# Kernel tuning notes

Hardware: AMD Instinct MI355X
Metric: run time of the kernel (lower is better)

## Reference

```python
import jax, jax.numpy as jnp
import numpy as np

B, N, IN_DIM, H, L = 8, 1024, 3, 256, 3
NUM_STEPS = 200
LN_EPS = 1e-5


def _cdist(a, b):
    # Euclidean pairwise distance, a:[B,n,d], b:[B,m,d] -> [B,n,m]
    d2 = (jnp.sum(a * a, -1)[:, :, None] + jnp.sum(b * b, -1)[:, None, :]
          - 2.0 * jnp.einsum('bik,bjk->bij', a, b))
    d2 = jnp.maximum(d2, 0.0)
    safe = jnp.sqrt(jnp.where(d2 > 0, d2, 1.0))
    return jnp.where(d2 > 0, safe, 0.0)


def _layernorm(x, g, b):
    mu = jnp.mean(x, -1, keepdims=True)
    var = jnp.mean(jnp.square(x - mu), -1, keepdims=True)
    return (x - mu) * jax.lax.rsqrt(var + LN_EPS) * g + b


def setup_inputs() -> dict:
    key = jax.random.key(0)
    ks = jax.random.split(key, 32)
    s = 0.02
    inp = {
        'x': jax.random.normal(ks[0], (B, N, IN_DIM), jnp.float32),
        't': jax.random.randint(ks[1], (B,), 0, NUM_STEPS),
        'mask': jnp.ones((B, N), bool),
        # top-level weights (stored [in,out])
        'w_time': jax.random.normal(ks[2], (1, H)) * s,
        'b_time': jnp.zeros((H,)),
        'w_in': jax.random.normal(ks[3], (IN_DIM + H, H)) * s,
        'b_in': jnp.zeros((H,)),
        'w_out': jax.random.normal(ks[4], (H, IN_DIM)) * s,
        'b_out': jnp.zeros((IN_DIM,)),
        # per-layer stacked params [L, ...]
        'qkv_w': jax.random.normal(ks[5], (L, H, 3 * H)) * s,
        'qkv_b': jnp.zeros((L, 3 * H)),
        'ao_w': jax.random.normal(ks[6], (L, H, H)) * s,
        'ao_b': jnp.zeros((L, H)),
        'fc1_w': jax.random.normal(ks[7], (L, H, 4 * H)) * s,
        'fc1_b': jax.random.normal(ks[8], (L, 4 * H)) * s,
        'fc2_w': jax.random.normal(ks[9], (L, 4 * H, H)) * s,
        'fc2_b': jax.random.normal(ks[10], (L, H)) * s,
        'ln1_g': jnp.ones((L, H)), 'ln1_b': jnp.zeros((L, H)),
        'ln2_g': jnp.ones((L, H)), 'ln2_b': jnp.zeros((L, H)),
    }
    return inp


def reference(x, t, mask, w_time, b_time, w_in, b_in, w_out, b_out,
              qkv_w, qkv_b, ao_w, ao_b, fc1_w, fc1_b, fc2_w, fc2_b,
              ln1_g, ln1_b, ln2_g, ln2_b):
    tf = t.astype(jnp.float32)[:, None] / float(NUM_STEPS)          # [B,1]
    t_embed = jax.nn.relu(tf @ w_time + b_time)                      # [B,H]
    t_embed = jnp.broadcast_to(t_embed[:, None, :], (B, N, H))
    h = jax.nn.relu(jnp.concatenate([x, t_embed], -1) @ w_in + b_in)  # [B,N,H]
    geo = _cdist(h[:, :, :3], h[:, :, :3])                           # [B,N,N]
    mask_f = mask.astype(h.dtype)
    scale = 1.0 / jnp.sqrt(jnp.float32(H))
    for l in range(L):
        qkv = (h @ qkv_w[l] + qkv_b[l]).reshape(B, N, 3, H)
        q, k, v = qkv[:, :, 0], qkv[:, :, 1], qkv[:, :, 2]
        dist = _cdist(geo, geo)                                      # cdist of the distance matrix itself
        scores = jnp.einsum('bik,bjk->bij', q, k) * scale * jnp.exp(-dist)
        scores = jnp.where(mask[:, None, :], scores, -jnp.inf)
        attn = jax.nn.softmax(scores, axis=-1)
        ao = (jnp.einsum('bij,bjk->bik', attn, v) @ ao_w[l] + ao_b[l]) * mask_f[:, :, None]
        xx = _layernorm(h + ao, ln1_g[l], ln1_b[l])
        f1 = jax.nn.relu((xx @ fc1_w[l] + fc1_b[l]) * mask_f[:, :, None])
        ffn = jax.nn.relu((f1 @ fc2_w[l] + fc2_b[l]) * mask_f[:, :, None])
        h = _layernorm(xx + ffn, ln2_g[l], ln2_b[l])
    return (h @ w_out + b_out) * mask_f[:, :, None]
```

## Files before the change

### kernel.cpp

```cpp
#include <hip/hip_runtime.h>
#include <math.h>

#define NB 8
#define NN 1024
#define NH 256
#define NL 3

typedef unsigned short u16;
typedef __bf16 bf16x8 __attribute__((ext_vector_type(8)));
typedef _Float16 f16x8 __attribute__((ext_vector_type(8)));
typedef float f32x4 __attribute__((ext_vector_type(4)));

constexpr int EPI_BIAS_RELU = 2, EPI_BIAS_RELU_RESID = 3, EPI_EDIST = 5, EPI_QKV = 6;

__device__ __forceinline__ unsigned bf16rne(float f) {
    unsigned u = __float_as_uint(f);
    return (u + 0x7fffu + ((u >> 16) & 1u)) >> 16;
}
__device__ __forceinline__ unsigned bfpair(float a, float b) {
    return bf16rne(a) | (bf16rne(b) << 16);
}
__device__ __forceinline__ float bf2f(u16 h) {
    unsigned u = ((unsigned)h) << 16;
    return __uint_as_float(u);
}

__device__ __forceinline__ float blockSum256(float v) {
    __shared__ float sm[4];
    #pragma unroll
    for (int o = 32; o; o >>= 1) v += __shfl_down(v, o, 64);
    int lane = threadIdx.x & 63, wid = threadIdx.x >> 6;
    if (lane == 0) sm[wid] = v;
    __syncthreads();
    if (threadIdx.x == 0) sm[0] = sm[0] + sm[1] + sm[2] + sm[3];
    __syncthreads();
    float r = sm[0];
    __syncthreads();
    return r;
}

template <int EPI, int DT, bool OBF, int SWZ, int MT>
__global__ __launch_bounds__(256) void gemm_mfma(
    const u16* __restrict__ A, int lda, long sA,
    const u16* __restrict__ Bt, int ldb, long sB,
    void* __restrict__ C, int ldc, long sC,
    int K,
    const float* __restrict__ bias, long sBias,
    const float* __restrict__ resid, int ldr,
    u16* __restrict__ vtout)
{
    constexpr int MF = MT / 32;
    constexpr int ASZ = MT * 8;
    __shared__ uint4 sm4[ASZ + 1024];
    const int tid = threadIdx.x;

    int bx = blockIdx.x, by = blockIdx.y, bz = blockIdx.z;
    bool trans = false;
    if (SWZ == 2) {
        int gx = gridDim.x;
        int T = gx * gridDim.y;
        int lid = bx + gx * by;
        int nl = (lid & 7) * (T >> 3) + (lid >> 3);
        bx = nl % gx; by = nl / gx;
    } else if (SWZ == 3) {
        int lid = bx + gridDim.x * bz;
        bz = lid & 7;
        int idx = lid >> 3;
        int j = 0;
        while (idx >= 16 - 2 * j) { idx -= 16 - 2 * j; j++; }
        by = 2 * j + idx;
        bx = j;
        trans = (by >= 2 * bx + 2);
    }
    const int z = bz;
    const int row0 = by * MT, col0 = bx * 128;

    f32x4 acc[MF][4];
    #pragma unroll
    for (int m = 0; m < MF; m++)
        #pragma unroll
        for (int n = 0; n < 4; n++) acc[m][n] = (f32x4){0.f, 0.f, 0.f, 0.f};

    const int l = tid & 63, wid = tid >> 6;
    const int wr = wid >> 1, wc = wid & 1;
    const int lrow = l & 15, lgrp = l >> 4;

    for (int k0 = 0; k0 < K; k0 += 64) {
        if (MT == 128) {
            const int srow = tid >> 1, half = tid & 1, cb = half * 4, swz = srow & 7;
            const u16* Ap = A + (long)z * sA + (long)(row0 + srow) * lda + k0 + half * 32;
            uint4 a0 = *(const uint4*)(Ap + 0),  a1 = *(const uint4*)(Ap + 8);
            uint4 a2 = *(const uint4*)(Ap + 16), a3 = *(const uint4*)(Ap + 24);
            sm4[srow * 8 + ((cb + 0) ^ swz)] = a0;
            sm4[srow * 8 + ((cb + 1) ^ swz)] = a1;
            sm4[srow * 8 + ((cb + 2) ^ swz)] = a2;
            sm4[srow * 8 + ((cb + 3) ^ swz)] = a3;
        } else {
            const int arow = tid >> 2, aq = tid & 3, swz = arow & 7;
            const u16* Ap = A + (long)z * sA + (long)(row0 + arow) * lda + k0 + aq * 16;
            uint4 a0 = *(const uint4*)(Ap + 0), a1 = *(const uint4*)(Ap + 8);
            sm4[arow * 8 + ((aq * 2 + 0) ^ swz)] = a0;
            sm4[arow * 8 + ((aq * 2 + 1) ^ swz)] = a1;
        }
        {
            const int brow = tid >> 1, bq = tid & 1, cb = bq * 4, swz = brow & 7;
            const u16* Bp = Bt + (long)z * sB + (long)(col0 + brow) * ldb + k0 + bq * 32;
            uint4 b0 = *(const uint4*)(Bp + 0),  b1 = *(const uint4*)(Bp + 8);
            uint4 b2 = *(const uint4*)(Bp + 16), b3 = *(const uint4*)(Bp + 24);
            sm4[ASZ + brow * 8 + ((cb + 0) ^ swz)] = b0;
            sm4[ASZ + brow * 8 + ((cb + 1) ^ swz)] = b1;
            sm4[ASZ + brow * 8 + ((cb + 2) ^ swz)] = b2;
            sm4[ASZ + brow * 8 + ((cb + 3) ^ swz)] = b3;
        }
        __syncthreads();

        #pragma unroll
        for (int ks = 0; ks < 2; ks++) {
            int c = ks * 4 + lgrp;
            uint4 a[MF], b[4];
            #pragma unroll
            for (int m = 0; m < MF; m++) {
                int r = wr * (MT / 2) + m * 16 + lrow;
                a[m] = sm4[r * 8 + (c ^ (r & 7))];
            }
            #pragma unroll
            for (int n = 0; n < 4; n++) {
                int r = wc * 64 + n * 16 + lrow;
                b[n] = sm4[ASZ + r * 8 + (c ^ (r & 7))];
            }
            #pragma unroll
            for (int m = 0; m < MF; m++)
                #pragma unroll
                for (int n = 0; n < 4; n++) {
                    if (DT == 0)
                        acc[m][n] = __builtin_amdgcn_mfma_f32_16x16x32_bf16(
                            __builtin_bit_cast(bf16x8, a[m]), __builtin_bit_cast(bf16x8, b[n]), acc[m][n], 0, 0, 0);
                    else
                        acc[m][n] = __builtin_amdgcn_mfma_f32_16x16x32_f16(
                            __builtin_bit_cast(f16x8, a[m]), __builtin_bit_cast(f16x8, b[n]), acc[m][n], 0, 0, 0);
                }
        }
        __syncthreads();
    }

    #pragma unroll
    for (int m = 0; m < MF; m++) {
        #pragma unroll
        for (int n = 0; n < 4; n++) {
            int rbase = row0 + wr * (MT / 2) + m * 16 + lgrp * 4;
            int cc = col0 + wc * 64 + n * 16 + lrow;
            float bv = 0.f;
            if (EPI == EPI_QKV || EPI == EPI_BIAS_RELU || EPI == EPI_BIAS_RELU_RESID)
                bv = bias[cc];
            float vals[4];
            #pragma unroll
            for (int reg = 0; reg < 4; reg++) {
                long r = rbase + reg;
                float v = acc[m][n][reg];
                if (EPI == EPI_QKV) v += bv;
                else if (EPI == EPI_BIAS_RELU) v = fmaxf(v + bv, 0.f);
                else if (EPI == EPI_BIAS_RELU_RESID) v = fmaxf(v + bv, 0.f) + resid[r * ldr + cc];
                else if (EPI == EPI_EDIST) {
                    const float* rnb = bias + (long)z * sBias;
                    float d2 = fmaxf(rnb[r] + rnb[cc] - 2.f * v, 0.f);
                    v = (r == cc) ? 1.f : expf(-sqrtf(d2));
                }
                vals[reg] = v;
                if (OBF) ((u16*)C)[(long)z * sC + r * ldc + cc] = (u16)bf16rne(v);
                else     ((float*)C)[(long)z * sC + r * ldc + cc] = v;
            }
            if (EPI == EPI_EDIST && SWZ == 3 && trans) {
                uint2 tv;
                tv.x = bfpair(vals[0], vals[1]);
                tv.y = bfpair(vals[2], vals[3]);
                *(uint2*)&((u16*)C)[(long)z * sC + (long)cc * ldc + rbase] = tv;
            }
            if (EPI == EPI_QKV && cc >= 512) {
                int b = rbase >> 10;
                uint2 tv;
                tv.x = bfpair(vals[0], vals[1]);
                tv.y = bfpair(vals[2], vals[3]);
                *(uint2*)&vtout[(long)b * NH * NN + (long)(cc - 512) * NN + (rbase & 1023)] = tv;
            }
        }
    }
}

__global__ __launch_bounds__(512) void flash_k(
    const u16* __restrict__ qkv,
    const u16* __restrict__ vt,
    const u16* __restrict__ edist,
    const u16* __restrict__ aow,
    const float* __restrict__ aob,
    const float* __restrict__ hres,
    const float* __restrict__ g1,
    const float* __restrict__ b1,
    float* __restrict__ xb,
    u16* __restrict__ xbbf,
    float scale)
{
    __shared__ uint4 Ks[128][32];
    __shared__ uint4 Vts[256][16];
    __shared__ __align__(16) u16 Es[32][136];
    __shared__ __align__(16) u16 Ps[32][136];
    __shared__ float rs[32][8];
    __shared__ float lnA[32][8];
    __shared__ float lnB[32][8];

    const int tid = threadIdx.x;
    const int l = tid & 63, w = tid >> 6;
    const int g = l >> 4, lr = l & 15;

    int lid = blockIdx.x + gridDim.x * blockIdx.y;
    const int b = lid & 7;
    const int q0 = (lid >> 3) * 32;

    const u16* qkvb = qkv + (long)b * NN * 768;
    const u16* vtb  = vt + (long)b * NH * NN;
    const u16* eb   = edist + (long)b * NN * NN;

    uint4 qf[2][8];
    #pragma unroll
    for (int m = 0; m < 2; m++)
        #pragma unroll
        for (int ks = 0; ks < 8; ks++)
            qf[m][ks] = *(const uint4*)(qkvb + (long)(q0 + 16 * m + lr) * 768 + 32 * ks + 8 * g);

    f32x4 oacc[2][2];
    #pragma unroll
    for (int m = 0; m < 2; m++)
        #pragma unroll
        for (int nf = 0; nf < 2; nf++) oacc[m][nf] = (f32x4){0.f, 0.f, 0.f, 0.f};
    float rsum[2][4] = {{0.f, 0.f, 0.f, 0.f}, {0.f, 0.f, 0.f, 0.f}};

    for (int n0 = 0; n0 < NN; n0 += 128) {
        #pragma unroll
        for (int i = 0; i < 8; i++) {
            int idx = tid + 512 * i;
            int row = idx >> 5, ch = idx & 31;
            Ks[row][ch ^ (row & 7)] = *(const uint4*)(qkvb + (long)(n0 + row) * 768 + 256 + ch * 8);
        }
        #pragma unroll
        for (int i = 0; i < 8; i++) {
            int idx = tid + 512 * i;
            int c = idx >> 4, ch = idx & 15;
            Vts[c][(ch & 8) | ((ch & 7) ^ (c & 7))] = *(const uint4*)(vtb + (long)c * NN + n0 + ch * 8);
        }
        {
            int r = tid >> 4, ch = tid & 15;
            *(uint4*)&Es[r][ch * 8] = *(const uint4*)(eb + (long)(q0 + r) * NN + n0 + ch * 8);
        }
        __syncthreads();

        f32x4 s[2];
        s[0] = (f32x4){0.f, 0.f, 0.f, 0.f};
        s[1] = (f32x4){0.f, 0.f, 0.f, 0.f};
        const int krow = w * 16 + lr;
        #pragma unroll
        for (int ks = 0; ks < 8; ks++) {
            bf16x8 kf = __builtin_bit_cast(bf16x8, Ks[krow][(4 * ks + g) ^ (krow & 7)]);
            s[0] = __builtin_amdgcn_mfma_f32_16x16x32_bf16(__builtin_bit_cast(bf16x8, qf[0][ks]), kf, s[0], 0, 0, 0);
            s[1] = __builtin_amdgcn_mfma_f32_16x16x32_bf16(__builtin_bit_cast(bf16x8, qf[1][ks]), kf, s[1], 0, 0, 0);
        }
        #pragma unroll
        for (int m = 0; m < 2; m++)
            #pragma unroll
            for (int reg = 0; reg < 4; reg++) {
                int q = 16 * m + 4 * g + reg;
                int kc = w * 16 + lr;
                float p = expf(s[m][reg] * scale * bf2f(Es[q][kc]));
                rsum[m][reg] += p;
                Ps[q][kc] = (u16)bf16rne(p);
            }
        __syncthreads();
        #pragma unroll
        for (int ks = 0; ks < 4; ks++) {
            bf16x8 pa[2], vbf[2];
            #pragma unroll
            for (int m = 0; m < 2; m++)
                pa[m] = __builtin_bit_cast(bf16x8, *(const uint4*)&Ps[16 * m + lr][32 * ks + 8 * g]);
            #pragma unroll
            for (int nf = 0; nf < 2; nf++) {
                int c = w * 32 + nf * 16 + lr;
                int ch = 4 * ks + g;
                vbf[nf] = __builtin_bit_cast(bf16x8, Vts[c][(ch & 8) | ((ch & 7) ^ (c & 7))]);
            }
            #pragma unroll
            for (int m = 0; m < 2; m++)
                #pragma unroll
                for (int nf = 0; nf < 2; nf++)
                    oacc[m][nf] = __builtin_amdgcn_mfma_f32_16x16x32_bf16(pa[m], vbf[nf], oacc[m][nf], 0, 0, 0);
        }
        __syncthreads();
    }

    #pragma unroll
    for (int m = 0; m < 2; m++)
        #pragma unroll
        for (int reg = 0; reg < 4; reg++) {
            float v = rsum[m][reg];
            v += __shfl_xor(v, 1); v += __shfl_xor(v, 2);
            v += __shfl_xor(v, 4); v += __shfl_xor(v, 8);
            rsum[m][reg] = v;
        }
    if (lr == 0) {
        #pragma unroll
        for (int m = 0; m < 2; m++)
            #pragma unroll
            for (int reg = 0; reg < 4; reg++)
                rs[16 * m + 4 * g + reg][w] = rsum[m][reg];
    }
    __syncthreads();

    u16* Os = (u16*)Ks;
    #pragma unroll
    for (int m = 0; m < 2; m++)
        #pragma unroll
        for (int reg = 0; reg < 4; reg++) {
            int q = 16 * m + 4 * g + reg;
            float t = 0.f;
            #pragma unroll
            for (int j = 0; j < 8; j++) t += rs[q][j];
            float inv = 1.f / t;
            #pragma unroll
            for (int nf = 0; nf < 2; nf++) {
                int c = w * 32 + nf * 16 + lr;
                Os[q * 264 + c] = (u16)bf16rne(oacc[m][nf][reg] * inv);
            }
        }
    __syncthreads();

    f32x4 aacc[2][2];
    #pragma unroll
    for (int m = 0; m < 2; m++)
        #pragma unroll
        for (int nf = 0; nf < 2; nf++) aacc[m][nf] = (f32x4){0.f, 0.f, 0.f, 0.f};
    #pragma unroll
    for (int kc = 0; kc < 8; kc++) {
        bf16x8 pa[2], wb[2];
        #pragma unroll
        for (int m = 0; m < 2; m++)
            pa[m] = __builtin_bit_cast(bf16x8, *(const uint4*)&Os[(16 * m + lr) * 264 + kc * 32 + 8 * g]);
        #pragma unroll
        for (int nf = 0; nf < 2; nf++)
            wb[nf] = __builtin_bit_cast(bf16x8, *(const uint4*)(aow + (long)(32 * w + 16 * nf + lr) * 256 + kc * 32 + 8 * g));
        #pragma unroll
        for (int m = 0; m < 2; m++)
            #pragma unroll
            for (int nf = 0; nf < 2; nf++)
                aacc[m][nf] = __builtin_amdgcn_mfma_f32_16x16x32_bf16(pa[m], wb[nf], aacc[m][nf], 0, 0, 0);
    }

    int j0 = 32 * w + lr, j1 = 32 * w + 16 + lr;
    float aob0 = aob[j0], aob1 = aob[j1];
    float xv[2][2][4];
    #pragma unroll
    for (int m = 0; m < 2; m++)
        #pragma unroll
        for (int reg = 0; reg < 4; reg++) {
            int q = 16 * m + 4 * g + reg;
            long hr = ((long)b * NN + q0 + q) * NH;
            xv[m][0][reg] = aacc[m][0][reg] + aob0 + hres[hr + j0];
            xv[m][1][reg] = aacc[m][1][reg] + aob1 + hres[hr + j1];
        }

    #pragma unroll
    for (int m = 0; m < 2; m++)
        #pragma unroll
        for (int reg = 0; reg < 4; reg++) {
            float s = xv[m][0][reg] + xv[m][1][reg];
            float s2 = xv[m][0][reg] * xv[m][0][reg] + xv[m][1][reg] * xv[m][1][reg];
            s  += __shfl_xor(s, 1);  s  += __shfl_xor(s, 2);  s  += __shfl_xor(s, 4);  s  += __shfl_xor(s, 8);
            s2 += __shfl_xor(s2, 1); s2 += __shfl_xor(s2, 2); s2 += __shfl_xor(s2, 4); s2 += __shfl_xor(s2, 8);
            if (lr == 0) {
                int q = 16 * m + 4 * g + reg;
                lnA[q][w] = s;
                lnB[q][w] = s2;
            }
        }
    __syncthreads();

    float g1v0 = g1[j0], g1v1 = g1[j1], b1v0 = b1[j0], b1v1 = b1[j1];
    #pragma unroll
    for (int m = 0; m < 2; m++)
        #pragma unroll
        for (int reg = 0; reg < 4; reg++) {
            int q = 16 * m + 4 * g + reg;
            float S = 0.f, S2 = 0.f;
            #pragma unroll
            for (int j = 0; j < 8; j++) { S += lnA[q][j]; S2 += lnB[q][j]; }
            float mu = S * (1.f / NH);
            float var = S2 * (1.f / NH) - mu * mu;
            float rsd = rsqrtf(var + 1e-5f);
            long hr = ((long)b * NN + q0 + q) * NH;
            float o0 = (xv[m][0][reg] - mu) * rsd * g1v0 + b1v0;
            float o1 = (xv[m][1][reg] - mu) * rsd * g1v1 + b1v1;
            xb[hr + j0] = o0;
            xb[hr + j1] = o1;
            xbbf[hr + j0] = (u16)bf16rne(o0);
            xbbf[hr + j1] = (u16)bf16rne(o1);
        }
}

__global__ __launch_bounds__(256) void base_k(const int* __restrict__ t,
                                              const float* __restrict__ w_time,
                                              const float* __restrict__ b_time,
                                              const float* __restrict__ w_in,
                                              const float* __restrict__ b_in,
                                              float* __restrict__ base) {
    int b = blockIdx.x, j = threadIdx.x;
    __shared__ float te[256];
    float tf = (float)t[b] / 200.0f;
    te[j] = fmaxf(tf * w_time[j] + b_time[j], 0.f);
    __syncthreads();
    float acc = b_in[j];
    for (int k = 0; k < 256; k++) acc = fmaf(te[k], w_in[(3 + k) * 256 + j], acc);
    base[b * 256 + j] = acc;
}

__global__ __launch_bounds__(256) void hinit_k(const float* __restrict__ x,
                                               const float* __restrict__ w_in,
                                               const float* __restrict__ base,
                                               float* __restrict__ h,
                                               u16* __restrict__ hbf,
                                               float* __restrict__ h3) {
    long row = blockIdx.x;
    int b = (int)(row >> 10);
    int j = threadIdx.x;
    float x0 = x[row * 3 + 0], x1 = x[row * 3 + 1], x2 = x[row * 3 + 2];
    float v = base[b * 256 + j];
    v = fmaf(x0, w_in[j], v);
    v = fmaf(x1, w_in[256 + j], v);
    v = fmaf(x2, w_in[512 + j], v);
    v = fmaxf(v, 0.f);
    h[row * 256 + j] = v;
    hbf[row * 256 + j] = (u16)bf16rne(v);
    if (j < 3) h3[row * 3 + j] = v;
}

__global__ __launch_bounds__(256) void geo_k(const float* __restrict__ h3,
                                             u16* __restrict__ gf,
                                             float* __restrict__ rn) {
    int bi = blockIdx.x;
    int b = bi >> 10, i = bi & 1023;
    const float* hb = h3 + (long)b * NN * 3;
    float ax = hb[i * 3 + 0], ay = hb[i * 3 + 1], az = hb[i * 3 + 2];
    u16* grow = gf + (long)bi * 1024;
    float accs = 0.f;
    #pragma unroll
    for (int j0 = 0; j0 < NN; j0 += 256) {
        int j = j0 + threadIdx.x;
        float dx = hb[j * 3 + 0] - ax, dy = hb[j * 3 + 1] - ay, dz = hb[j * 3 + 2] - az;
        float d2 = dx * dx + dy * dy + dz * dz;
        float d = (d2 > 0.f) ? sqrtf(d2) : 0.f;
        _Float16 hf = (_Float16)d;
        float rep = (float)hf;
        grow[j] = __builtin_bit_cast(u16, hf);
        accs += rep * rep;
    }
    float tot = blockSum256(accs);
    if (threadIdx.x == 0) rn[bi] = tot;
}

__global__ __launch_bounds__(256) void wtrans_k(const float* __restrict__ qkv_w,
                                                const float* __restrict__ ao_w,
                                                const float* __restrict__ fc1_w,
                                                const float* __restrict__ fc2_w,
                                                u16* __restrict__ qkv_wt,
                                                u16* __restrict__ ao_wt,
                                                u16* __restrict__ fc1_wt,
                                                u16* __restrict__ fc2_wt) {
    int type = blockIdx.z, lyr = blockIdx.y;
    int R, Cc;
    const float* src;
    u16* dst;
    if (type == 0) { R = 256; Cc = 768;  src = qkv_w + (long)lyr * R * Cc; dst = qkv_wt + (long)lyr * R * Cc; }
    else if (type == 1) { R = 256; Cc = 256; src = ao_w + (long)lyr * R * Cc; dst = ao_wt + (long)lyr * R * Cc; }
    else if (type == 2) { R = 256; Cc = 1024; src = fc1_w + (long)lyr * R * Cc; dst = fc1_wt + (long)lyr * R * Cc; }
    else { R = 1024; Cc = 256; src = fc2_w + (long)lyr * R * Cc; dst = fc2_wt + (long)lyr * R * Cc; }
    int tC = Cc >> 5, tR = R >> 5;
    int tile = blockIdx.x;
    if (tile >= tC * tR) return;
    int c0 = (tile % tC) << 5, r0 = (tile / tC) << 5;
    __shared__ float tf[32][33];
    int tx = threadIdx.x & 31, ty = threadIdx.x >> 5;
    #pragma unroll
    for (int i = 0; i < 4; i++) {
        int r = ty + 8 * i;
        tf[r][tx] = src[(long)(r0 + r) * Cc + c0 + tx];
    }
    __syncthreads();
    #pragma unroll
    for (int i = 0; i < 4; i++) {
        int c = ty + 8 * i;
        dst[(long)(c0 + c) * R + r0 + tx] = (u16)bf16rne(tf[tx][c]);
    }
}

__global__ __launch_bounds__(256) void ln_k(float* __restrict__ X,
                                            u16* __restrict__ Xbf,
                                            const float* __restrict__ g,
                                            const float* __restrict__ b) {
    int wid = threadIdx.x >> 6, l = threadIdx.x & 63;
    long row = (long)blockIdx.x * 4 + wid;
    float* p = X + row * NH;
    float4 v = *(float4*)(p + l * 4);
    float s = v.x + v.y + v.z + v.w;
    #pragma unroll
    for (int o = 32; o; o >>= 1) s += __shfl_xor(s, o);
    float mu = s * (1.f / NH);
    float4 d = {v.x - mu, v.y - mu, v.z - mu, v.w - mu};
    float q = d.x * d.x + d.y * d.y + d.z * d.z + d.w * d.w;
    #pragma unroll
    for (int o = 32; o; o >>= 1) q += __shfl_xor(q, o);
    float rsd = rsqrtf(q * (1.f / NH) + 1e-5f);
    float4 g4 = *(const float4*)(g + l * 4);
    float4 b4 = *(const float4*)(b + l * 4);
    float4 o4;
    o4.x = d.x * rsd * g4.x + b4.x;
    o4.y = d.y * rsd * g4.y + b4.y;
    o4.z = d.z * rsd * g4.z + b4.z;
    o4.w = d.w * rsd * g4.w + b4.w;
    *(float4*)(p + l * 4) = o4;
    uint2 pk;
    pk.x = bfpair(o4.x, o4.y);
    pk.y = bfpair(o4.z, o4.w);
    *(uint2*)(Xbf + row * NH + l * 4) = pk;
}

__global__ __launch_bounds__(256) void out_k(const float* __restrict__ h,
                                             const float* __restrict__ w_out,
                                             const float* __restrict__ b_out,
                                             float* __restrict__ out) {
    long row = blockIdx.x;
    int wid = threadIdx.x >> 6, lane = threadIdx.x & 63;
    if (wid < 3) {
        float acc = 0.f;
        for (int k = lane; k < 256; k += 64) acc = fmaf(h[row * 256 + k], w_out[k * 3 + wid], acc);
        #pragma unroll
        for (int o = 32; o; o >>= 1) acc += __shfl_down(acc, o, 64);
        if (lane == 0) out[row * 3 + wid] = acc + b_out[wid];
    }
}

extern "C" void kernel_launch(void* const* d_in, const int* in_sizes, int n_in,
                              void* d_out, int out_size, void* d_ws, size_t ws_size,
                              hipStream_t stream) {
    const float* x      = (const float*)d_in[0];
    const int*   t      = (const int*)  d_in[1];
    const float* w_time = (const float*)d_in[3];
    const float* b_time = (const float*)d_in[4];
    const float* w_in   = (const float*)d_in[5];
    const float* b_in   = (const float*)d_in[6];
    const float* w_out  = (const float*)d_in[7];
    const float* b_out  = (const float*)d_in[8];
    const float* qkv_w  = (const float*)d_in[9];
    const float* qkv_b  = (const float*)d_in[10];
    const float* ao_w   = (const float*)d_in[11];
    const float* ao_b   = (const float*)d_in[12];
    const float* fc1_w  = (const float*)d_in[13];
    const float* fc1_b  = (const float*)d_in[14];
    const float* fc2_w  = (const float*)d_in[15];
    const float* fc2_b  = (const float*)d_in[16];
    const float* ln1_g  = (const float*)d_in[17];
    const float* ln1_b  = (const float*)d_in[18];
    const float* ln2_g  = (const float*)d_in[19];
    const float* ln2_b  = (const float*)d_in[20];
    float* out = (float*)d_out;

    char* W = (char*)d_ws;
    float* h     = (float*)(W);
    float* xb    = (float*)(W + (8ul << 20));
    u16*   hbf   = (u16*)  (W + (16ul << 20));
    u16*   xbbf  = (u16*)  (W + (20ul << 20));
    u16*   vt    = (u16*)  (W + (24ul << 20));
    u16*   f1    = (u16*)  (W + (28ul << 20));
    u16*   qkvb  = (u16*)  (W + (44ul << 20));
    u16*   edist = (u16*)  (W + (56ul << 20));
    u16*   gf    = (u16*)  (W + (72ul << 20));
    u16*   wts   = (u16*)  (W + (88ul << 20));
    u16* qkv_wt = wts;
    u16* ao_wt  = wts + 589824;
    u16* fc1_wt = wts + 786432;
    u16* fc2_wt = wts + 1572864;
    float* base = (float*)(W + (94ul << 20));
    float* rn   = base + 2048;
    float* h3   = rn + 8192;

    const float scale = 1.0f / 16.0f;

    base_k<<<NB, 256, 0, stream>>>(t, w_time, b_time, w_in, b_in, base);
    hinit_k<<<NB * NN, 256, 0, stream>>>(x, w_in, base, h, hbf, h3);
    geo_k<<<NB * NN, 256, 0, stream>>>(h3, gf, rn);
    wtrans_k<<<dim3(256, NL, 4), 256, 0, stream>>>(qkv_w, ao_w, fc1_w, fc2_w,
                                                   qkv_wt, ao_wt, fc1_wt, fc2_wt);
    gemm_mfma<EPI_EDIST, 1, true, 3, 64><<<dim3(72, 1, 8), 256, 0, stream>>>(
        gf, 1024, (long)NN * 1024, gf, 1024, (long)NN * 1024,
        edist, NN, (long)NN * NN, 1024, rn, NN, nullptr, 0, nullptr);

    for (int l = 0; l < NL; ++l) {
        gemm_mfma<EPI_QKV, 0, true, 2, 128><<<dim3(6, 64, 1), 256, 0, stream>>>(
            hbf, NH, 0, qkv_wt + (long)l * 196608, NH, 0, qkvb, 768, 0,
            NH, qkv_b + l * 768, 0, nullptr, 0, vt);
        flash_k<<<dim3(32, 8), 512, 0, stream>>>(
            qkvb, vt, edist, ao_wt + (long)l * 65536, ao_b + l * NH,
            h, ln1_g + l * NH, ln1_b + l * NH, xb, xbbf, scale);
        gemm_mfma<EPI_BIAS_RELU, 0, true, 2, 128><<<dim3(8, 64, 1), 256, 0, stream>>>(
            xbbf, NH, 0, fc1_wt + (long)l * 262144, NH, 0, f1, 1024, 0,
            NH, fc1_b + l * 1024, 0, nullptr, 0, nullptr);
        gemm_mfma<EPI_BIAS_RELU_RESID, 0, false, 2, 64><<<dim3(2, 128, 1), 256, 0, stream>>>(
            f1, 1024, 0, fc2_wt + (long)l * 262144, 1024, 0, h, NH, 0,
            1024, fc2_b + l * NH, 0, xb, NH, nullptr);
        ln_k<<<2048, 256, 0, stream>>>(h, hbf, ln2_g + l * NH, ln2_b + l * NH);
    }
    out_k<<<NB * NN, 256, 0, stream>>>(h, w_out, b_out, out);
}
```

Before: 330.2 us.

## Fuse FFN (fc1, fc2, residual, LayerNorm) into one kernel; stage transposed edist stores

Replaces the separate fc1 GEMM, fc2 GEMM and LayerNorm kernels with one ffn_k kernel. Each 32-row block keeps its 32x1024 bf16 fc1 activations in shared memory, so the f1 buffer never makes a round trip through global memory and two launches go away. Each block also reads weights straight from global without tiling, and only 256 blocks run. Separately, the transposed edist write now goes through shared memory so the global stores are coalesced 16-byte writes instead of scattered 8-byte ones.

Measured after the change: 357.0 us. 8.1% more time.

```diff
diff --git a/kernel.cpp b/kernel.cpp
--- a/kernel.cpp
+++ b/kernel.cpp
@@ -11,7 +11,7 @@
 typedef _Float16 f16x8 __attribute__((ext_vector_type(8)));
 typedef float f32x4 __attribute__((ext_vector_type(4)));
 
-constexpr int EPI_BIAS_RELU = 2, EPI_BIAS_RELU_RESID = 3, EPI_EDIST = 5, EPI_QKV = 6;
+constexpr int EPI_EDIST = 5, EPI_QKV = 6;
 
 __device__ __forceinline__ unsigned bf16rne(float f) {
     unsigned u = __float_as_uint(f);
@@ -46,7 +46,6 @@
     void* __restrict__ C, int ldc, long sC,
     int K,
     const float* __restrict__ bias, long sBias,
-    const float* __restrict__ resid, int ldr,
     u16* __restrict__ vtout)
 {
     constexpr int MF = MT / 32;
@@ -143,6 +142,7 @@
         __syncthreads();
     }
 
+    u16* Ts = (u16*)sm4;
     #pragma unroll
     for (int m = 0; m < MF; m++) {
         #pragma unroll
@@ -150,16 +150,13 @@
             int rbase = row0 + wr * (MT / 2) + m * 16 + lgrp * 4;
             int cc = col0 + wc * 64 + n * 16 + lrow;
             float bv = 0.f;
-            if (EPI == EPI_QKV || EPI == EPI_BIAS_RELU || EPI == EPI_BIAS_RELU_RESID)
-                bv = bias[cc];
+            if (EPI == EPI_QKV) bv = bias[cc];
             float vals[4];
             #pragma unroll
             for (int reg = 0; reg < 4; reg++) {
                 long r = rbase + reg;
                 float v = acc[m][n][reg];
                 if (EPI == EPI_QKV) v += bv;
-                else if (EPI == EPI_BIAS_RELU) v = fmaxf(v + bv, 0.f);
-                else if (EPI == EPI_BIAS_RELU_RESID) v = fmaxf(v + bv, 0.f) + resid[r * ldr + cc];
                 else if (EPI == EPI_EDIST) {
                     const float* rnb = bias + (long)z * sBias;
                     float d2 = fmaxf(rnb[r] + rnb[cc] - 2.f * v, 0.f);
@@ -170,10 +167,11 @@
                 else     ((float*)C)[(long)z * sC + r * ldc + cc] = v;
             }
             if (EPI == EPI_EDIST && SWZ == 3 && trans) {
+                int cl = cc - col0, rl = rbase - row0;
                 uint2 tv;
                 tv.x = bfpair(vals[0], vals[1]);
                 tv.y = bfpair(vals[2], vals[3]);
-                *(uint2*)&((u16*)C)[(long)z * sC + (long)cc * ldc + rbase] = tv;
+                *(uint2*)(Ts + cl * 68 + rl) = tv;
             }
             if (EPI == EPI_QKV && cc >= 512) {
                 int b = rbase >> 10;
@@ -183,6 +181,21 @@
                 *(uint2*)&vtout[(long)b * NH * NN + (long)(cc - 512) * NN + (rbase & 1023)] = tv;
             }
         }
+    }
+    if (EPI == EPI_EDIST && SWZ == 3 && trans) {
+        __syncthreads();
+        int row = tid >> 1, half = tid & 1;
+        const u16* src = Ts + row * 68 + half * 32;
+        uint2 v0 = *(const uint2*)(src + 0),  v1 = *(const uint2*)(src + 4);
+        uint2 v2 = *(const uint2*)(src + 8),  v3 = *(const uint2*)(src + 12);
+        uint2 v4 = *(const uint2*)(src + 16), v5 = *(const uint2*)(src + 20);
+        uint2 v6 = *(const uint2*)(src + 24), v7 = *(const uint2*)(src + 28);
+        uint4* dst = (uint4*)((u16*)C + (long)z * sC + (long)(col0 + row) * ldc + row0 + half * 32);
+        uint4 w0 = {v0.x, v0.y, v1.x, v1.y};
+        uint4 w1 = {v2.x, v2.y, v3.x, v3.y};
+        uint4 w2 = {v4.x, v4.y, v5.x, v5.y};
+        uint4 w3 = {v6.x, v6.y, v7.x, v7.y};
+        dst[0] = w0; dst[1] = w1; dst[2] = w2; dst[3] = w3;
     }
 }
 
@@ -400,6 +413,152 @@
             xbbf[hr + j0] = (u16)bf16rne(o0);
             xbbf[hr + j1] = (u16)bf16rne(o1);
         }
+}
+
+__global__ __launch_bounds__(512) void ffn_k(
+    const u16* __restrict__ X,
+    const float* __restrict__ resid,
+    const u16* __restrict__ w1,
+    const float* __restrict__ b1,
+    const u16* __restrict__ w2,
+    const float* __restrict__ b2,
+    const float* __restrict__ g2,
+    const float* __restrict__ bb2,
+    float* __restrict__ hout,
+    u16* __restrict__ hbf)
+{
+    __shared__ __align__(16) u16 f1s[32 * 1024];
+    __shared__ float lnA[32][8], lnB[32][8];
+
+    const int tid = threadIdx.x;
+    const int l = tid & 63, w = tid >> 6;
+    const int g = l >> 4, lr = l & 15;
+    const long r0 = (long)blockIdx.x * 32;
+
+    uint4 bx[2][8];
+    #pragma unroll
+    for (int nf = 0; nf < 2; nf++)
+        #pragma unroll
+        for (int kc = 0; kc < 8; kc++)
+            bx[nf][kc] = *(const uint4*)(X + (r0 + 16 * nf + lr) * 256 + 32 * kc + 8 * g);
+
+    f32x4 acc1[8][2];
+    #pragma unroll
+    for (int m = 0; m < 8; m++)
+        #pragma unroll
+        for (int nf = 0; nf < 2; nf++) acc1[m][nf] = (f32x4){0.f, 0.f, 0.f, 0.f};
+    #pragma unroll
+    for (int kc = 0; kc < 8; kc++) {
+        #pragma unroll
+        for (int m = 0; m < 8; m++) {
+            bf16x8 a = __builtin_bit_cast(bf16x8,
+                *(const uint4*)(w1 + (long)(128 * w + 16 * m + lr) * 256 + 32 * kc + 8 * g));
+            acc1[m][0] = __builtin_amdgcn_mfma_f32_16x16x32_bf16(a, __builtin_bit_cast(bf16x8, bx[0][kc]), acc1[m][0], 0, 0, 0);
+            acc1[m][1] = __builtin_amdgcn_mfma_f32_16x16x32_bf16(a, __builtin_bit_cast(bf16x8, bx[1][kc]), acc1[m][1], 0, 0, 0);
+        }
+    }
+    #pragma unroll
+    for (int m = 0; m < 8; m++) {
+        float4 bv = *(const float4*)(b1 + 128 * w + 16 * m + 4 * g);
+        int c4 = 16 * w + 2 * m + (g >> 1);
+        #pragma unroll
+        for (int nf = 0; nf < 2; nf++) {
+            int q = 16 * nf + lr;
+            float v0 = fmaxf(acc1[m][nf][0] + bv.x, 0.f);
+            float v1 = fmaxf(acc1[m][nf][1] + bv.y, 0.f);
+            float v2 = fmaxf(acc1[m][nf][2] + bv.z, 0.f);
+            float v3 = fmaxf(acc1[m][nf][3] + bv.w, 0.f);
+            uint2 pk;
+            pk.x = bfpair(v0, v1);
+            pk.y = bfpair(v2, v3);
+            ((uint2*)f1s)[q * 256 + (c4 ^ (q & 7)) * 2 + (g & 1)] = pk;
+        }
+    }
+    __syncthreads();
+
+    f32x4 acc2[2][2];
+    #pragma unroll
+    for (int m = 0; m < 2; m++)
+        #pragma unroll
+        for (int nf = 0; nf < 2; nf++) acc2[m][nf] = (f32x4){0.f, 0.f, 0.f, 0.f};
+    #pragma unroll
+    for (int kc = 0; kc < 32; kc++) {
+        bf16x8 bq[2];
+        #pragma unroll
+        for (int nf = 0; nf < 2; nf++) {
+            int q = 16 * nf + lr;
+            bq[nf] = __builtin_bit_cast(bf16x8, ((const uint4*)f1s)[q * 128 + ((4 * kc + g) ^ (q & 7))]);
+        }
+        #pragma unroll
+        for (int m = 0; m < 2; m++) {
+            bf16x8 a = __builtin_bit_cast(bf16x8,
+                *(const uint4*)(w2 + (long)(32 * w + 16 * m + lr) * 1024 + 32 * kc + 8 * g));
+            acc2[m][0] = __builtin_amdgcn_mfma_f32_16x16x32_bf16(a, bq[0], acc2[m][0], 0, 0, 0);
+            acc2[m][1] = __builtin_amdgcn_mfma_f32_16x16x32_bf16(a, bq[1], acc2[m][1], 0, 0, 0);
+        }
+    }
+
+    float xv[2][2][4];
+    #pragma unroll
+    for (int m = 0; m < 2; m++) {
+        float4 bv = *(const float4*)(b2 + 32 * w + 16 * m + 4 * g);
+        #pragma unroll
+        for (int nf = 0; nf < 2; nf++) {
+            int q = 16 * nf + lr;
+            const float* rp = resid + (r0 + q) * 256 + 32 * w + 16 * m + 4 * g;
+            float4 rv = *(const float4*)rp;
+            xv[m][nf][0] = fmaxf(acc2[m][nf][0] + bv.x, 0.f) + rv.x;
+            xv[m][nf][1] = fmaxf(acc2[m][nf][1] + bv.y, 0.f) + rv.y;
+            xv[m][nf][2] = fmaxf(acc2[m][nf][2] + bv.z, 0.f) + rv.z;
+            xv[m][nf][3] = fmaxf(acc2[m][nf][3] + bv.w, 0.f) + rv.w;
+        }
+    }
+
+    #pragma unroll
+    for (int nf = 0; nf < 2; nf++) {
+        float s = 0.f, s2 = 0.f;
+        #pragma unroll
+        for (int m = 0; m < 2; m++)
+            #pragma unroll
+            for (int reg = 0; reg < 4; reg++) {
+                s += xv[m][nf][reg];
+                s2 += xv[m][nf][reg] * xv[m][nf][reg];
+            }
+        s  += __shfl_xor(s, 16);  s  += __shfl_xor(s, 32);
+        s2 += __shfl_xor(s2, 16); s2 += __shfl_xor(s2, 32);
+        if (g == 0) {
+            lnA[16 * nf + lr][w] = s;
+            lnB[16 * nf + lr][w] = s2;
+        }
+    }
+    __syncthreads();
+
+    #pragma unroll
+    for (int nf = 0; nf < 2; nf++) {
+        int q = 16 * nf + lr;
+        float S = 0.f, S2 = 0.f;
+        #pragma unroll
+        for (int j = 0; j < 8; j++) { S += lnA[q][j]; S2 += lnB[q][j]; }
+        float mu = S * (1.f / NH);
+        float var = S2 * (1.f / NH) - mu * mu;
+        float rsd = rsqrtf(var + 1e-5f);
+        #pragma unroll
+        for (int m = 0; m < 2; m++) {
+            int cb = 32 * w + 16 * m + 4 * g;
+            float4 g4 = *(const float4*)(g2 + cb);
+            float4 b4 = *(const float4*)(bb2 + cb);
+            float o0 = (xv[m][nf][0] - mu) * rsd * g4.x + b4.x;
+            float o1 = (xv[m][nf][1] - mu) * rsd * g4.y + b4.y;
+            float o2 = (xv[m][nf][2] - mu) * rsd * g4.z + b4.z;
+            float o3 = (xv[m][nf][3] - mu) * rsd * g4.w + b4.w;
+            float4 o4 = {o0, o1, o2, o3};
+            *(float4*)(hout + (r0 + q) * 256 + cb) = o4;
+            uint2 pk;
+            pk.x = bfpair(o0, o1);
+            pk.y = bfpair(o2, o3);
+            *(uint2*)(hbf + (r0 + q) * 256 + cb) = pk;
+        }
+    }
 }
 
 __global__ __launch_bounds__(256) void base_k(const int* __restrict__ t,
@@ -495,37 +654,6 @@
         int c = ty + 8 * i;
         dst[(long)(c0 + c) * R + r0 + tx] = (u16)bf16rne(tf[tx][c]);
     }
-}
-
-__global__ __launch_bounds__(256) void ln_k(float* __restrict__ X,
-                                            u16* __restrict__ Xbf,
-                                            const float* __restrict__ g,
-                                            const float* __restrict__ b) {
-    int wid = threadIdx.x >> 6, l = threadIdx.x & 63;
-    long row = (long)blockIdx.x * 4 + wid;
-    float* p = X + row * NH;
-    float4 v = *(float4*)(p + l * 4);
-    float s = v.x + v.y + v.z + v.w;
-    #pragma unroll
-    for (int o = 32; o; o >>= 1) s += __shfl_xor(s, o);
-    float mu = s * (1.f / NH);
-    float4 d = {v.x - mu, v.y - mu, v.z - mu, v.w - mu};
-    float q = d.x * d.x + d.y * d.y + d.z * d.z + d.w * d.w;
-    #pragma unroll
-    for (int o = 32; o; o >>= 1) q += __shfl_xor(q, o);
-    float rsd = rsqrtf(q * (1.f / NH) + 1e-5f);
-    float4 g4 = *(const float4*)(g + l * 4);
-    float4 b4 = *(const float4*)(b + l * 4);
-    float4 o4;
-    o4.x = d.x * rsd * g4.x + b4.x;
-    o4.y = d.y * rsd * g4.y + b4.y;
-    o4.z = d.z * rsd * g4.z + b4.z;
-    o4.w = d.w * rsd * g4.w + b4.w;
-    *(float4*)(p + l * 4) = o4;
-    uint2 pk;
-    pk.x = bfpair(o4.x, o4.y);
-    pk.y = bfpair(o4.z, o4.w);
-    *(uint2*)(Xbf + row * NH + l * 4) = pk;
 }
 
 __global__ __launch_bounds__(256) void out_k(const float* __restrict__ h,
@@ -574,16 +702,15 @@
     u16*   hbf   = (u16*)  (W + (16ul << 20));
     u16*   xbbf  = (u16*)  (W + (20ul << 20));
     u16*   vt    = (u16*)  (W + (24ul << 20));
-    u16*   f1    = (u16*)  (W + (28ul << 20));
-    u16*   qkvb  = (u16*)  (W + (44ul << 20));
-    u16*   edist = (u16*)  (W + (56ul << 20));
-    u16*   gf    = (u16*)  (W + (72ul << 20));
-    u16*   wts   = (u16*)  (W + (88ul << 20));
+    u16*   qkvb  = (u16*)  (W + (28ul << 20));
+    u16*   edist = (u16*)  (W + (40ul << 20));
+    u16*   gf    = (u16*)  (W + (56ul << 20));
+    u16*   wts   = (u16*)  (W + (72ul << 20));
     u16* qkv_wt = wts;
     u16* ao_wt  = wts + 589824;
     u16* fc1_wt = wts + 786432;
     u16* fc2_wt = wts + 1572864;
-    float* base = (float*)(W + (94ul << 20));
+    float* base = (float*)(W + (78ul << 20));
     float* rn   = base + 2048;
     float* h3   = rn + 8192;
 
@@ -596,22 +723,19 @@
                                                    qkv_wt, ao_wt, fc1_wt, fc2_wt);
     gemm_mfma<EPI_EDIST, 1, true, 3, 64><<<dim3(72, 1, 8), 256, 0, stream>>>(
         gf, 1024, (long)NN * 1024, gf, 1024, (long)NN * 1024,
-        edist, NN, (long)NN * NN, 1024, rn, NN, nullptr, 0, nullptr);
+        edist, NN, (long)NN * NN, 1024, rn, NN, nullptr);
 
     for (int l = 0; l < NL; ++l) {
         gemm_mfma<EPI_QKV, 0, true, 2, 128><<<dim3(6, 64, 1), 256, 0, stream>>>(
             hbf, NH, 0, qkv_wt + (long)l * 196608, NH, 0, qkvb, 768, 0,
-            NH, qkv_b + l * 768, 0, nullptr, 0, vt);
+            NH, qkv_b + l * 768, 0, vt);
         flash_k<<<dim3(32, 8), 512, 0, stream>>>(
             qkvb, vt, edist, ao_wt + (long)l * 65536, ao_b + l * NH,
             h, ln1_g + l * NH, ln1_b + l * NH, xb, xbbf, scale);
-        gemm_mfma<EPI_BIAS_RELU, 0, true, 2, 128><<<dim3(8, 64, 1), 256, 0, stream>>>(
-            xbbf, NH, 0, fc1_wt + (long)l * 262144, NH, 0, f1, 1024, 0,
-            NH, fc1_b + l * 1024, 0, nullptr, 0, nullptr);
-        gemm_mfma<EPI_BIAS_RELU_RESID, 0, false, 2, 64><<<dim3(2, 128, 1), 256, 0, stream>>>(
-            f1, 1024, 0, fc2_wt + (long)l * 262144, 1024, 0, h, NH, 0,
-            1024, fc2_b + l * NH, 0, xb, NH, nullptr);
-        ln_k<<<2048, 256, 0, stream>>>(h, hbf, ln2_g + l * NH, ln2_b + l * NH);
+        ffn_k<<<256, 512, 0, stream>>>(
+            xbbf, xb, fc1_wt + (long)l * 262144, fc1_b + l * 1024,
+            fc2_wt + (long)l * 262144, fc2_b + l * NH,
+            ln2_g + l * NH, ln2_b + l * NH, h, hbf);
     }
     out_k<<<NB * NN, 256, 0, stream>>>(h, w_out, b_out, out);
 }
```
